# Optimization experiments

Measured on AMD Instinct MI355X. Metric: run time of the kernel, lower is better.

Reference implementation:

```python
import jax, jax.numpy as jnp
import numpy as np

T_TYPES = 4      # node types
N_NODES = 8192   # nodes per type
D_IN = 256       # init_dim
H = 256          # hidden_dim
D_OUT = 64       # out_dim
N_LAYERS = 2     # args.trans_num
TEMP = 1.0       # args.search_temp


def _conv1d(x, w, b):
    # x: [T, N, Din] -> Conv1d over node axis (torch: data[j].T -> Conv1d -> .T)
    # w: [Dout, Din, 3], b: [Dout]
    y = jax.lax.conv_general_dilated(
        jnp.swapaxes(x, 1, 2), w, window_strides=(1,), padding=((1, 1),),
        dimension_numbers=('NCH', 'OIH', 'NCH'))
    return jnp.swapaxes(y + b[None, :, None], 1, 2)  # [T, N, Dout]


def _rel_conv1d(x, w, b):
    # per-type conv kernels: w [T, Dout, Din, 3], b [T, Dout]
    return jax.vmap(lambda xi, wi, bi: _conv1d(xi[None], wi, bi)[0])(x, w, b)


def setup_inputs() -> dict:
    key = jax.random.key(0)
    ks = jax.random.split(key, 16)
    s = 1.0 / np.sqrt(H)  # keep relu chains numerically tame
    return {
        'x': jax.random.normal(ks[0], (T_TYPES, N_NODES, D_IN), jnp.float32),
        'lin1_w': jax.random.normal(ks[1], (D_IN, H), jnp.float32) * s,
        'lin1_b': jax.random.normal(ks[2], (H,), jnp.float32) * 0.01,
        'lin_w': jax.random.normal(ks[3], (N_LAYERS, H, H), jnp.float32) * s,
        'lin_b': jax.random.normal(ks[4], (N_LAYERS, H), jnp.float32) * 0.01,
        'rel_lin_w': jax.random.normal(ks[5], (N_LAYERS, T_TYPES, H, H), jnp.float32) * s,
        'rel_lin_b': jax.random.normal(ks[6], (N_LAYERS, T_TYPES, H), jnp.float32) * 0.01,
        'conv_w': jax.random.normal(ks[7], (N_LAYERS, H, H, 3), jnp.float32) * s,
        'conv_b': jax.random.normal(ks[8], (N_LAYERS, H), jnp.float32) * 0.01,
        'rel_conv_w': jax.random.normal(ks[9], (N_LAYERS, T_TYPES, H, H, 3), jnp.float32) * s,
        'rel_conv_b': jax.random.normal(ks[10], (N_LAYERS, T_TYPES, H), jnp.float32) * 0.01,
        'out_w': jax.random.normal(ks[11], (H, D_OUT), jnp.float32) * s,
        'out_b': jax.random.normal(ks[12], (D_OUT,), jnp.float32) * 0.01,
        'trans_arch': jax.random.normal(ks[13], (N_LAYERS, 5), jnp.float32),
        'agg_arch': jax.random.normal(ks[14], (3,), jnp.float32),
    }


def reference(x, lin1_w, lin1_b, lin_w, lin_b, rel_lin_w, rel_lin_b,
              conv_w, conv_b, rel_conv_w, rel_conv_b, out_w, out_b,
              trans_arch, agg_arch):
    relu = jax.nn.relu
    tw = jax.nn.softmax(trans_arch / TEMP, axis=-1)  # [L, 5]
    aw = jax.nn.softmax(agg_arch / TEMP)             # [3]

    # input projection (lin1)
    h = jnp.einsum('tnd,de->tne', x, lin1_w) + lin1_b  # [T, N, H]

    for l in range(N_LAYERS):
        # TRANS_OPTION = ['linear','rel-linear','conv','rel-conv','identity']
        o_lin = relu(jnp.einsum('tnd,de->tne', h, lin_w[l]) + lin_b[l])
        o_rlin = relu(jnp.einsum('tnd,tde->tne', h, rel_lin_w[l]) + rel_lin_b[l][:, None, :])
        o_conv = relu(_conv1d(h, conv_w[l], conv_b[l]))
        o_rconv = relu(_rel_conv1d(h, rel_conv_w[l], rel_conv_b[l]))
        w = tw[l]
        h = w[0] * o_lin + w[1] * o_rlin + w[2] * o_conv + w[3] * o_rconv + w[4] * h

    # Agg_Op: concat all types along node axis, AGG_OPTION = ['sum','mean','max']
    flat = h.reshape(-1, H)  # [T*N, H]
    agg = aw[0] * flat.sum(axis=0) + aw[1] * flat.mean(axis=0) + aw[2] * flat.max(axis=0)

    # reconstructed output head (class body truncated in source)
    return agg @ out_w + out_b  # [D_OUT]
```

## Files before the change

### kernel.cpp

```cpp
#include <hip/hip_runtime.h>
#include <hip/hip_bf16.h>
#include <math.h>

#define NN 8192
#define HP 8194
#define HD 256
#define DOUT 64

typedef __bf16 bf16_t;
typedef __bf16 bf16x8 __attribute__((ext_vector_type(8)));
typedef float f32x4 __attribute__((ext_vector_type(4)));

#define H0_OFF 0ull
#define H1_OFF 16781312ull
#define PW_OFF 33562624ull
#define TW_OFF 38936576ull
#define PS_OFF 38936832ull
#define PM_OFF 39198976ull
#define PWG_L1 0
#define PWG_SH(l) (8192 + (l)*32768)
#define PWG_TY(l) (73728 + (l)*131072)

__device__ __forceinline__ void glds16(const void* g, void* l) {
    __builtin_amdgcn_global_load_lds(
        (const __attribute__((address_space(1))) void*)g,
        (__attribute__((address_space(3))) void*)l, 16, 0, 0);
}

__device__ __forceinline__ float frelu(float v) { return v > 0.f ? v : 0.f; }

__global__ __launch_bounds__(256) void pack_kernel(
    const float* __restrict__ lin1_w, const float* __restrict__ lin_w,
    const float* __restrict__ rel_lin_w, const float* __restrict__ conv_w,
    const float* __restrict__ rel_conv_w, const float* __restrict__ trans_arch,
    const float* __restrict__ agg_arch, bf16_t* __restrict__ pw,
    float* __restrict__ tws, bf16_t* __restrict__ h0, bf16_t* __restrict__ h1) {
    const int bxi = blockIdx.x;
    if (bxi < 1312) {
        int g = bxi * 256 + threadIdx.x;
        int lrow = g & 15, lq = (g >> 4) & 3, j2 = (g >> 6) & 3;
        float v[8];
        if (g < 8192) {
            int ct = (g >> 8) & 3, kt = g >> 10;
            int k = kt * 32 + lq * 8, n = ct * 64 + j2 * 16 + lrow;
#pragma unroll
            for (int e = 0; e < 8; ++e) v[e] = lin1_w[(k + e) * 256 + n];
        } else if (g < 73728) {
            int u = g - 8192; int l = u >> 15; int r = u & 32767;
            int s = (r >> 8) & 3, ct = (r >> 10) & 3, kt = r >> 12;
            int k = kt * 32 + lq * 8, n = ct * 64 + j2 * 16 + lrow;
            if (s == 0) {
#pragma unroll
                for (int e = 0; e < 8; ++e) v[e] = lin_w[(l * 256 + k + e) * 256 + n];
            } else {
#pragma unroll
                for (int e = 0; e < 8; ++e)
                    v[e] = conv_w[((l * 256 + n) * 256 + k + e) * 3 + (s - 1)];
            }
        } else {
            int u = g - 73728; int lt = u >> 15; int l = lt >> 2, tt = lt & 3;
            int r = u & 32767;
            int s = (r >> 8) & 3, ct = (r >> 10) & 3, kt = r >> 12;
            int k = kt * 32 + lq * 8, n = ct * 64 + j2 * 16 + lrow;
            if (s == 0) {
#pragma unroll
                for (int e = 0; e < 8; ++e)
                    v[e] = rel_lin_w[((l * 4 + tt) * 256 + k + e) * 256 + n];
            } else {
#pragma unroll
                for (int e = 0; e < 8; ++e)
                    v[e] = rel_conv_w[(((l * 4 + tt) * 256 + n) * 256 + k + e) * 3 + (s - 1)];
            }
        }
        bf16x8 wv;
#pragma unroll
        for (int e = 0; e < 8; ++e) wv[e] = (bf16_t)v[e];
        *(bf16x8*)(pw + (size_t)g * 8) = wv;
    } else if (bxi == 1312) {
        for (int idx = threadIdx.x; idx < 4096; idx += 256) {
            int row_id = idx >> 8, col = idx & 255;
            int buf = row_id >> 3, t_ = (row_id >> 1) & 3, side = row_id & 1;
            bf16_t* hb = buf ? h1 : h0;
            hb[((size_t)t_ * HP + (side ? (HP - 1) : 0)) * HD + col] = (bf16_t)0.f;
        }
    } else {
        if (threadIdx.x == 0) {
            for (int l = 0; l < 2; ++l) {
                float m = trans_arch[l * 5];
                for (int i = 1; i < 5; ++i) m = fmaxf(m, trans_arch[l * 5 + i]);
                float e[5], s = 0.f;
                for (int i = 0; i < 5; ++i) { e[i] = __expf(trans_arch[l * 5 + i] - m); s += e[i]; }
                for (int i = 0; i < 5; ++i) tws[l * 5 + i] = e[i] / s;
            }
            float m = fmaxf(fmaxf(agg_arch[0], agg_arch[1]), agg_arch[2]);
            float e0 = __expf(agg_arch[0] - m), e1 = __expf(agg_arch[1] - m), e2 = __expf(agg_arch[2] - m);
            float s = e0 + e1 + e2;
            tws[10] = e0 / s; tws[11] = e1 / s; tws[12] = e2 / s;
        }
    }
}

__device__ __forceinline__ void load_af(bf16x8 af[4], const bf16_t* lA,
                                        int sh, int wm, int lrow, int lq) {
#pragma unroll
    for (int i = 0; i < 4; ++i)
        af[i] = *(const bf16x8*)&lA[(sh + wm + i * 16 + lrow) * 40 + lq * 8];
}

__device__ __forceinline__ void do_mat(const bf16x8 af[4], const bf16_t* Bb,
                                       int grpbase, int lane, f32x4 acc[4][2]) {
#pragma unroll
    for (int j = 0; j < 2; ++j) {
        bf16x8 bfr = *(const bf16x8*)&Bb[(grpbase + j) * 512 + lane * 8];
#pragma unroll
        for (int i = 0; i < 4; ++i)
            acc[i][j] = __builtin_amdgcn_mfma_f32_16x16x32_bf16(af[i], bfr, acc[i][j], 0, 0, 0);
    }
}

__global__ __launch_bounds__(256, 2) void lin1_kernel(
    const float* __restrict__ x, bf16_t* __restrict__ h0,
    const bf16_t* __restrict__ pwL1, const float* __restrict__ b) {
    __shared__ __align__(16) bf16_t lA[128 * 40];
    __shared__ __align__(16) bf16_t lB[2][2048];
    const int tid = threadIdx.x, lane = tid & 63, wid = tid >> 6;
    const int bx = blockIdx.x;
    const int t = bx >> 8, rb = bx & 255, mt = rb >> 2, ct = rb & 3;
    const int m0 = mt * 128, c0 = ct * 64;
    const int wm = (wid >> 1) * 64, wn = (wid & 1) * 32;
    const int lrow = lane & 15, lq = lane >> 4;
    const int wj2 = wn >> 4;
    const int r0 = tid >> 1, kq0 = (tid & 1) * 2;
    const float* xT = x + (size_t)t * NN * HD + (size_t)(m0 + r0) * HD + kq0 * 8;

    f32x4 acc[4][2];
#pragma unroll
    for (int i = 0; i < 4; ++i)
#pragma unroll
        for (int j = 0; j < 2; ++j) acc[i][j] = (f32x4){0.f, 0.f, 0.f, 0.f};

    float4 xa0, xa1, xa2, xa3;
    {
        const float4* p = (const float4*)(xT);
        xa0 = p[0]; xa1 = p[1]; xa2 = p[2]; xa3 = p[3];
    }
    {
        const bf16_t* src = pwL1 + (size_t)((0 * 4 + ct) * 4 + wid) * 512 + (size_t)lane * 8;
        glds16(src, &lB[0][wid * 512]);
    }
    for (int kt = 0; kt < 8; ++kt) {
        bf16x8 w0, w1;
        w0[0]=(bf16_t)xa0.x; w0[1]=(bf16_t)xa0.y; w0[2]=(bf16_t)xa0.z; w0[3]=(bf16_t)xa0.w;
        w0[4]=(bf16_t)xa1.x; w0[5]=(bf16_t)xa1.y; w0[6]=(bf16_t)xa1.z; w0[7]=(bf16_t)xa1.w;
        w1[0]=(bf16_t)xa2.x; w1[1]=(bf16_t)xa2.y; w1[2]=(bf16_t)xa2.z; w1[3]=(bf16_t)xa2.w;
        w1[4]=(bf16_t)xa3.x; w1[5]=(bf16_t)xa3.y; w1[6]=(bf16_t)xa3.z; w1[7]=(bf16_t)xa3.w;
        *(bf16x8*)&lA[r0 * 40 + kq0 * 8] = w0;
        *(bf16x8*)&lA[r0 * 40 + kq0 * 8 + 8] = w1;
        if (kt < 7) {
            const float4* p = (const float4*)(xT + (kt + 1) * 32);
            xa0 = p[0]; xa1 = p[1]; xa2 = p[2]; xa3 = p[3];
        }
        __syncthreads();
        if (kt < 7) {
            const bf16_t* src = pwL1 + (size_t)(((kt + 1) * 4 + ct) * 4 + wid) * 512 + (size_t)lane * 8;
            glds16(src, &lB[(kt + 1) & 1][wid * 512]);
        }
        const bf16_t* Bb = lB[kt & 1];
        bf16x8 af[4];
        load_af(af, lA, 0, wm, lrow, lq);
#pragma unroll
        for (int j = 0; j < 2; ++j) {
            bf16x8 bfr = *(const bf16x8*)&Bb[(wj2 + j) * 512 + lane * 8];
#pragma unroll
            for (int i = 0; i < 4; ++i)
                acc[i][j] = __builtin_amdgcn_mfma_f32_16x16x32_bf16(af[i], bfr, acc[i][j], 0, 0, 0);
        }
        __syncthreads();
    }
    size_t obase = (size_t)t * HP * HD + (size_t)(1 + m0) * HD;
#pragma unroll
    for (int j = 0; j < 2; ++j) {
        int col = c0 + wn + j * 16 + lrow;
        float bj = b[col];
#pragma unroll
        for (int i = 0; i < 4; ++i)
#pragma unroll
            for (int r = 0; r < 4; ++r) {
                int orow = wm + i * 16 + lq * 4 + r;
                h0[obase + (size_t)orow * HD + col] = (bf16_t)(acc[i][j][r] + bj);
            }
    }
}

__global__ __launch_bounds__(256, 2) void layer_kernel(
    const bf16_t* __restrict__ hin, bf16_t* __restrict__ hout,
    const bf16_t* __restrict__ pwS, const bf16_t* __restrict__ pwT,
    const float* __restrict__ lin_b, const float* __restrict__ rel_lin_b,
    const float* __restrict__ conv_b, const float* __restrict__ rel_conv_b,
    const float* __restrict__ tw5) {
    __shared__ __align__(16) bf16_t lA[130 * 40];
    __shared__ __align__(16) bf16_t lB[2][16384];
    const int tid = threadIdx.x, lane = tid & 63, wid = tid >> 6;
    const int bx = blockIdx.x;
    const int t = bx >> 8, rb = bx & 255, mt = rb >> 2, ct = rb & 3;
    const int m0 = mt * 128, c0 = ct * 64;
    const int wm = (wid >> 1) * 64, wn = (wid & 1) * 32;
    const int lrow = lane & 15, lq = lane >> 4;
    const int wj2 = wn >> 4;
    const bf16_t* aG = hin + (size_t)t * HP * HD + (size_t)m0 * HD;
    const bf16_t* pwTt = pwT + (size_t)t * 262144;
    const int r0 = tid >> 1, kq0 = (tid & 1) * 2;
    const int r1 = 128 + (tid >> 1);
    const bool tail = (tid < 4);

    f32x4 acc[4][4][2];
#pragma unroll
    for (int m = 0; m < 4; ++m)
#pragma unroll
        for (int i = 0; i < 4; ++i)
#pragma unroll
            for (int j = 0; j < 2; ++j) acc[m][i][j] = (f32x4){0.f, 0.f, 0.f, 0.f};

    bf16x8 pa0, pa1, pb0, pb1;
    pa0 = *(const bf16x8*)(aG + (size_t)r0 * HD + kq0 * 8);
    pa1 = *(const bf16x8*)(aG + (size_t)r0 * HD + kq0 * 8 + 8);
    if (tail) {
        pb0 = *(const bf16x8*)(aG + (size_t)r1 * HD + kq0 * 8);
        pb1 = *(const bf16x8*)(aG + (size_t)r1 * HD + kq0 * 8 + 8);
    }
#pragma unroll
    for (int q = 0; q < 8; ++q) {
        int tk = wid * 8 + q, half = tk >> 4, grp = tk & 15;
        const bf16_t* src = (half ? pwTt : pwS) + (size_t)((0 * 4 + ct) * 16 + grp) * 512 + (size_t)lane * 8;
        glds16(src, &lB[0][(half * 16 + grp) * 512]);
    }
    for (int kt = 0; kt < 8; ++kt) {
        *(bf16x8*)&lA[r0 * 40 + kq0 * 8] = pa0;
        *(bf16x8*)&lA[r0 * 40 + kq0 * 8 + 8] = pa1;
        if (tail) {
            *(bf16x8*)&lA[r1 * 40 + kq0 * 8] = pb0;
            *(bf16x8*)&lA[r1 * 40 + kq0 * 8 + 8] = pb1;
        }
        if (kt < 7) {
            pa0 = *(const bf16x8*)(aG + (size_t)r0 * HD + (kt + 1) * 32 + kq0 * 8);
            pa1 = *(const bf16x8*)(aG + (size_t)r0 * HD + (kt + 1) * 32 + kq0 * 8 + 8);
            if (tail) {
                pb0 = *(const bf16x8*)(aG + (size_t)r1 * HD + (kt + 1) * 32 + kq0 * 8);
                pb1 = *(const bf16x8*)(aG + (size_t)r1 * HD + (kt + 1) * 32 + kq0 * 8 + 8);
            }
        }
        __syncthreads();
        if (kt < 7) {
            int buf = (kt + 1) & 1;
#pragma unroll
            for (int q = 0; q < 8; ++q) {
                int tk = wid * 8 + q, half = tk >> 4, grp = tk & 15;
                const bf16_t* src = (half ? pwTt : pwS) + (size_t)(((kt + 1) * 4 + ct) * 16 + grp) * 512 + (size_t)lane * 8;
                glds16(src, &lB[buf][(half * 16 + grp) * 512]);
            }
        }
        const bf16_t* Bb = lB[kt & 1];
        bf16x8 af[4];
        load_af(af, lA, 1, wm, lrow, lq);
        do_mat(af, Bb, 0 + 0 + wj2, lane, acc[0]);
        do_mat(af, Bb, 16 + 0 + wj2, lane, acc[1]);
        do_mat(af, Bb, 0 + 8 + wj2, lane, acc[2]);
        do_mat(af, Bb, 16 + 8 + wj2, lane, acc[3]);
        load_af(af, lA, 0, wm, lrow, lq);
        do_mat(af, Bb, 0 + 4 + wj2, lane, acc[2]);
        do_mat(af, Bb, 16 + 4 + wj2, lane, acc[3]);
        load_af(af, lA, 2, wm, lrow, lq);
        do_mat(af, Bb, 0 + 12 + wj2, lane, acc[2]);
        do_mat(af, Bb, 16 + 12 + wj2, lane, acc[3]);
        __syncthreads();
    }
    const float w0 = tw5[0], w1 = tw5[1], w2 = tw5[2], w3 = tw5[3], w4 = tw5[4];
    const float* rb1 = rel_lin_b + t * 256;
    const float* rb3 = rel_conv_b + t * 256;
    size_t obase = (size_t)t * HP * HD + (size_t)(1 + m0) * HD;
#pragma unroll
    for (int j = 0; j < 2; ++j) {
        int col = c0 + wn + j * 16 + lrow;
        float b0 = lin_b[col], b1 = rb1[col], b2 = conv_b[col], b3 = rb3[col];
#pragma unroll
        for (int i = 0; i < 4; ++i)
#pragma unroll
            for (int r = 0; r < 4; ++r) {
                int orow = wm + i * 16 + lq * 4 + r;
                size_t idx = obase + (size_t)orow * HD + col;
                float v = w0 * frelu(acc[0][i][j][r] + b0)
                        + w1 * frelu(acc[1][i][j][r] + b1)
                        + w2 * frelu(acc[2][i][j][r] + b2)
                        + w3 * frelu(acc[3][i][j][r] + b3)
                        + w4 * (float)hin[idx];
                hout[idx] = (bf16_t)v;
            }
    }
}

__global__ __launch_bounds__(256) void reduce1_kernel(
    const bf16_t* __restrict__ h, float* __restrict__ ps, float* __restrict__ pm) {
    __shared__ float ss[2048], sm[2048];
    const int tid = threadIdx.x, b = blockIdx.x;
    const int t = b >> 6, rblk = b & 63;
    const int cg = tid & 31, rs = tid >> 5;
    const bf16_t* base = h + ((size_t)t * HP + 1 + rblk * 128) * HD + cg * 8;
    float s[8], m[8];
#pragma unroll
    for (int j = 0; j < 8; ++j) { s[j] = 0.f; m[j] = -3.4e38f; }
    for (int ii = 0; ii < 16; ++ii) {
        bf16x8 v = *(const bf16x8*)(base + (size_t)(rs + ii * 8) * HD);
#pragma unroll
        for (int j = 0; j < 8; ++j) {
            float f = (float)v[j];
            s[j] += f; m[j] = fmaxf(m[j], f);
        }
    }
#pragma unroll
    for (int j = 0; j < 8; ++j) { ss[rs * 256 + cg * 8 + j] = s[j]; sm[rs * 256 + cg * 8 + j] = m[j]; }
    __syncthreads();
    int c = tid;
    float S = 0.f, M = -3.4e38f;
#pragma unroll
    for (int r = 0; r < 8; ++r) { S += ss[r * 256 + c]; M = fmaxf(M, sm[r * 256 + c]); }
    ps[c * 256 + b] = S;
    pm[c * 256 + b] = M;
}

__global__ void reduce2_kernel(const float* __restrict__ ps, const float* __restrict__ pm,
                               const float* __restrict__ out_w, const float* __restrict__ out_b,
                               const float* __restrict__ tws, float* __restrict__ out) {
    __shared__ float aggL[256];
    int c = threadIdx.x;
    float s = 0.f, m = -3.4e38f;
    const float4* p4 = (const float4*)(ps + (size_t)c * 256);
    const float4* q4 = (const float4*)(pm + (size_t)c * 256);
    for (int i = 0; i < 64; ++i) {
        float4 a = p4[i]; s += a.x + a.y + a.z + a.w;
        float4 b = q4[i]; m = fmaxf(m, fmaxf(fmaxf(b.x, b.y), fmaxf(b.z, b.w)));
    }
    float aw0 = tws[10], aw1 = tws[11], aw2 = tws[12];
    aggL[c] = aw0 * s + aw1 * (s * (1.0f / 32768.f)) + aw2 * m;
    __syncthreads();
    if (c < DOUT) {
        float o = out_b[c];
        for (int e = 0; e < 256; ++e) o += aggL[e] * out_w[e * DOUT + c];
        out[c] = o;
    }
}

extern "C" void kernel_launch(void* const* d_in, const int* in_sizes, int n_in,
                              void* d_out, int out_size, void* d_ws, size_t ws_size,
                              hipStream_t stream) {
    const float* x          = (const float*)d_in[0];
    const float* lin1_w     = (const float*)d_in[1];
    const float* lin1_b     = (const float*)d_in[2];
    const float* lin_w      = (const float*)d_in[3];
    const float* lin_b      = (const float*)d_in[4];
    const float* rel_lin_w  = (const float*)d_in[5];
    const float* rel_lin_b  = (const float*)d_in[6];
    const float* conv_w     = (const float*)d_in[7];
    const float* conv_b     = (const float*)d_in[8];
    const float* rel_conv_w = (const float*)d_in[9];
    const float* rel_conv_b = (const float*)d_in[10];
    const float* out_w      = (const float*)d_in[11];
    const float* out_b      = (const float*)d_in[12];
    const float* trans_arch = (const float*)d_in[13];
    const float* agg_arch   = (const float*)d_in[14];

    char* ws = (char*)d_ws;
    bf16_t* h0 = (bf16_t*)(ws + H0_OFF);
    bf16_t* h1 = (bf16_t*)(ws + H1_OFF);
    bf16_t* pw = (bf16_t*)(ws + PW_OFF);
    float* tws = (float*)(ws + TW_OFF);
    float* ps  = (float*)(ws + PS_OFF);
    float* pm  = (float*)(ws + PM_OFF);
    float* outp = (float*)d_out;

    pack_kernel<<<1314, 256, 0, stream>>>(lin1_w, lin_w, rel_lin_w, conv_w, rel_conv_w,
                                          trans_arch, agg_arch, pw, tws, h0, h1);
    lin1_kernel<<<1024, 256, 0, stream>>>(x, h0, pw + (size_t)PWG_L1 * 8, lin1_b);
    layer_kernel<<<1024, 256, 0, stream>>>(h0, h1,
        pw + (size_t)PWG_SH(0) * 8, pw + (size_t)PWG_TY(0) * 8,
        lin_b, rel_lin_b, conv_b, rel_conv_b, tws);
    layer_kernel<<<1024, 256, 0, stream>>>(h1, h0,
        pw + (size_t)PWG_SH(1) * 8, pw + (size_t)PWG_TY(1) * 8,
        lin_b + 256, rel_lin_b + 1024, conv_b + 256, rel_conv_b + 1024, tws + 5);
    reduce1_kernel<<<256, 256, 0, stream>>>(h0, ps, pm);
    reduce2_kernel<<<1, 256, 0, stream>>>(ps, pm, out_w, out_b, tws, outp);
}
```

Before: 234.0 us.

## Fuse reduction into last layer, coalesce weight packing, restructure lin1 and buffering

Weight packing now stages tiles through shared memory so global reads are coalesced, replacing strided per-element gathers. This cuts the pack grid from 1314 blocks to 410. The lin1 kernel now computes a full 64x256 output tile per block, so x is read once rather than four times. The layer kernel drops LDS double-buffering to single-buffered B in order to raise occupancy to 3 blocks per CU, which exposes the weight load latency. The second layer also computes per-block column sums and maxes in its epilogue, removing the separate reduce1 pass over h.

After: 331.4 us. 41.6% more time.

```diff
diff --git a/kernel.cpp b/kernel.cpp
--- a/kernel.cpp
+++ b/kernel.cpp
@@ -35,56 +35,76 @@
     const float* __restrict__ rel_conv_w, const float* __restrict__ trans_arch,
     const float* __restrict__ agg_arch, bf16_t* __restrict__ pw,
     float* __restrict__ tws, bf16_t* __restrict__ h0, bf16_t* __restrict__ h1) {
-    const int bxi = blockIdx.x;
-    if (bxi < 1312) {
-        int g = bxi * 256 + threadIdx.x;
-        int lrow = g & 15, lq = (g >> 4) & 3, j2 = (g >> 6) & 3;
-        float v[8];
-        if (g < 8192) {
-            int ct = (g >> 8) & 3, kt = g >> 10;
-            int k = kt * 32 + lq * 8, n = ct * 64 + j2 * 16 + lrow;
-#pragma unroll
-            for (int e = 0; e < 8; ++e) v[e] = lin1_w[(k + e) * 256 + n];
-        } else if (g < 73728) {
-            int u = g - 8192; int l = u >> 15; int r = u & 32767;
-            int s = (r >> 8) & 3, ct = (r >> 10) & 3, kt = r >> 12;
-            int k = kt * 32 + lq * 8, n = ct * 64 + j2 * 16 + lrow;
-            if (s == 0) {
-#pragma unroll
-                for (int e = 0; e < 8; ++e) v[e] = lin_w[(l * 256 + k + e) * 256 + n];
-            } else {
-#pragma unroll
-                for (int e = 0; e < 8; ++e)
-                    v[e] = conv_w[((l * 256 + n) * 256 + k + e) * 3 + (s - 1)];
-            }
-        } else {
-            int u = g - 73728; int lt = u >> 15; int l = lt >> 2, tt = lt & 3;
-            int r = u & 32767;
-            int s = (r >> 8) & 3, ct = (r >> 10) & 3, kt = r >> 12;
-            int k = kt * 32 + lq * 8, n = ct * 64 + j2 * 16 + lrow;
-            if (s == 0) {
-#pragma unroll
-                for (int e = 0; e < 8; ++e)
-                    v[e] = rel_lin_w[((l * 4 + tt) * 256 + k + e) * 256 + n];
-            } else {
-#pragma unroll
-                for (int e = 0; e < 8; ++e)
-                    v[e] = rel_conv_w[(((l * 4 + tt) * 256 + n) * 256 + k + e) * 3 + (s - 1)];
-            }
-        }
-        bf16x8 wv;
-#pragma unroll
-        for (int e = 0; e < 8; ++e) wv[e] = (bf16_t)v[e];
-        *(bf16x8*)(pw + (size_t)g * 8) = wv;
-    } else if (bxi == 1312) {
-        for (int idx = threadIdx.x; idx < 4096; idx += 256) {
-            int row_id = idx >> 8, col = idx & 255;
+    __shared__ float lt[32 * 257];
+    const int tid = threadIdx.x, bx = blockIdx.x;
+    if (bx < 88) {
+        int m = bx >> 3, kt = bx & 7;
+        const float* src; size_t img; bool l1 = (m == 0);
+        if (m == 0) { src = lin1_w; img = 0; }
+        else if (m <= 2) { int l = m - 1; src = lin_w + (size_t)l * 65536; img = PWG_SH(l); }
+        else { int u = m - 3; int l = u >> 2, tt = u & 3;
+            src = rel_lin_w + (size_t)(l * 4 + tt) * 65536;
+            img = PWG_TY(l) + (size_t)tt * 32768; }
+        const float4* s4 = (const float4*)(src + (size_t)kt * 32 * 256);
+#pragma unroll
+        for (int i = 0; i < 8; ++i) {
+            int idx = tid + 256 * i;
+            float4 v = s4[idx];
+            int k = idx >> 6, n = (idx * 4) & 255;
+            float* p = &lt[k * 257 + n];
+            p[0] = v.x; p[1] = v.y; p[2] = v.z; p[3] = v.w;
+        }
+        __syncthreads();
+        int j2 = tid >> 6, lq = (tid >> 4) & 3, lrow = tid & 15;
+#pragma unroll
+        for (int ct = 0; ct < 4; ++ct) {
+            int n = ct * 64 + j2 * 16 + lrow;
+            bf16x8 wv;
+#pragma unroll
+            for (int e = 0; e < 8; ++e) wv[e] = (bf16_t)lt[(lq * 8 + e) * 257 + n];
+            size_t g = l1 ? (img + (size_t)kt * 1024 + ct * 256 + tid)
+                          : (img + (size_t)kt * 4096 + ct * 1024 + tid);
+            *(bf16x8*)(pw + g * 8) = wv;
+        }
+    } else if (bx < 408) {
+        int idx = bx - 88;
+        int inst = idx >> 5, r = idx & 31, kt = r >> 2, ct = r & 3;
+        const float* src; size_t img;
+        if (inst < 2) { src = conv_w + (size_t)inst * 196608; img = PWG_SH(inst); }
+        else { int u = inst - 2; int l = u >> 2, tt = u & 3;
+            src = rel_conv_w + (size_t)(l * 4 + tt) * 196608;
+            img = PWG_TY(l) + (size_t)tt * 32768; }
+        {
+            int rl = tid >> 2, q0 = tid & 3;
+            int n = ct * 64 + rl;
+            const float4* rb = (const float4*)(src) + (size_t)n * 192 + kt * 24;
+#pragma unroll
+            for (int i = 0; i < 6; ++i) {
+                float4 v = rb[q0 + 4 * i];
+                float* p = &lt[rl * 100 + (q0 + 4 * i) * 4];
+                p[0] = v.x; p[1] = v.y; p[2] = v.z; p[3] = v.w;
+            }
+        }
+        __syncthreads();
+        int j2 = tid >> 6, lq = (tid >> 4) & 3, lrow = tid & 15;
+        int nl = j2 * 16 + lrow;
+#pragma unroll
+        for (int s = 1; s <= 3; ++s) {
+            bf16x8 wv;
+#pragma unroll
+            for (int e = 0; e < 8; ++e) wv[e] = (bf16_t)lt[nl * 100 + (lq * 8 + e) * 3 + (s - 1)];
+            size_t g = img + (size_t)kt * 4096 + ct * 1024 + s * 256 + tid;
+            *(bf16x8*)(pw + g * 8) = wv;
+        }
+    } else if (bx == 408) {
+        for (int i = tid; i < 4096; i += 256) {
+            int row_id = i >> 8, col = i & 255;
             int buf = row_id >> 3, t_ = (row_id >> 1) & 3, side = row_id & 1;
             bf16_t* hb = buf ? h1 : h0;
             hb[((size_t)t_ * HP + (side ? (HP - 1) : 0)) * HD + col] = (bf16_t)0.f;
         }
     } else {
-        if (threadIdx.x == 0) {
+        if (tid == 0) {
             for (int l = 0; l < 2; ++l) {
                 float m = trans_arch[l * 5];
                 for (int i = 1; i < 5; ++i) m = fmaxf(m, trans_arch[l * 5 + i]);
@@ -121,85 +141,78 @@
 __global__ __launch_bounds__(256, 2) void lin1_kernel(
     const float* __restrict__ x, bf16_t* __restrict__ h0,
     const bf16_t* __restrict__ pwL1, const float* __restrict__ b) {
-    __shared__ __align__(16) bf16_t lA[128 * 40];
-    __shared__ __align__(16) bf16_t lB[2][2048];
+    __shared__ __align__(16) bf16_t lA[64 * 40];
+    __shared__ __align__(16) bf16_t lB[8192];
     const int tid = threadIdx.x, lane = tid & 63, wid = tid >> 6;
     const int bx = blockIdx.x;
-    const int t = bx >> 8, rb = bx & 255, mt = rb >> 2, ct = rb & 3;
-    const int m0 = mt * 128, c0 = ct * 64;
-    const int wm = (wid >> 1) * 64, wn = (wid & 1) * 32;
+    const int t = bx >> 7, mt = bx & 127;
+    const int m0 = mt * 64;
     const int lrow = lane & 15, lq = lane >> 4;
-    const int wj2 = wn >> 4;
-    const int r0 = tid >> 1, kq0 = (tid & 1) * 2;
+    const int r0 = tid >> 2, kq0 = tid & 3;
     const float* xT = x + (size_t)t * NN * HD + (size_t)(m0 + r0) * HD + kq0 * 8;
 
-    f32x4 acc[4][2];
+    f32x4 acc[4][4];
 #pragma unroll
     for (int i = 0; i < 4; ++i)
 #pragma unroll
-        for (int j = 0; j < 2; ++j) acc[i][j] = (f32x4){0.f, 0.f, 0.f, 0.f};
-
-    float4 xa0, xa1, xa2, xa3;
-    {
-        const float4* p = (const float4*)(xT);
-        xa0 = p[0]; xa1 = p[1]; xa2 = p[2]; xa3 = p[3];
-    }
-    {
-        const bf16_t* src = pwL1 + (size_t)((0 * 4 + ct) * 4 + wid) * 512 + (size_t)lane * 8;
-        glds16(src, &lB[0][wid * 512]);
-    }
+        for (int j = 0; j < 4; ++j) acc[i][j] = (f32x4){0.f, 0.f, 0.f, 0.f};
+
+    float4 px0, px1;
+    { const float4* p = (const float4*)xT; px0 = p[0]; px1 = p[1]; }
+
     for (int kt = 0; kt < 8; ++kt) {
-        bf16x8 w0, w1;
-        w0[0]=(bf16_t)xa0.x; w0[1]=(bf16_t)xa0.y; w0[2]=(bf16_t)xa0.z; w0[3]=(bf16_t)xa0.w;
-        w0[4]=(bf16_t)xa1.x; w0[5]=(bf16_t)xa1.y; w0[6]=(bf16_t)xa1.z; w0[7]=(bf16_t)xa1.w;
-        w1[0]=(bf16_t)xa2.x; w1[1]=(bf16_t)xa2.y; w1[2]=(bf16_t)xa2.z; w1[3]=(bf16_t)xa2.w;
-        w1[4]=(bf16_t)xa3.x; w1[5]=(bf16_t)xa3.y; w1[6]=(bf16_t)xa3.z; w1[7]=(bf16_t)xa3.w;
-        *(bf16x8*)&lA[r0 * 40 + kq0 * 8] = w0;
-        *(bf16x8*)&lA[r0 * 40 + kq0 * 8 + 8] = w1;
+        __syncthreads();
+        bf16x8 wv;
+        wv[0]=(bf16_t)px0.x; wv[1]=(bf16_t)px0.y; wv[2]=(bf16_t)px0.z; wv[3]=(bf16_t)px0.w;
+        wv[4]=(bf16_t)px1.x; wv[5]=(bf16_t)px1.y; wv[6]=(bf16_t)px1.z; wv[7]=(bf16_t)px1.w;
+        *(bf16x8*)&lA[r0 * 40 + kq0 * 8] = wv;
+#pragma unroll
+        for (int j2 = 0; j2 < 4; ++j2) {
+            const bf16_t* src = pwL1 + ((size_t)kt * 1024 + wid * 256 + j2 * 64) * 8 + (size_t)lane * 8;
+            glds16(src, &lB[(wid * 4 + j2) * 512]);
+        }
         if (kt < 7) {
             const float4* p = (const float4*)(xT + (kt + 1) * 32);
-            xa0 = p[0]; xa1 = p[1]; xa2 = p[2]; xa3 = p[3];
-        }
-        __syncthreads();
-        if (kt < 7) {
-            const bf16_t* src = pwL1 + (size_t)(((kt + 1) * 4 + ct) * 4 + wid) * 512 + (size_t)lane * 8;
-            glds16(src, &lB[(kt + 1) & 1][wid * 512]);
-        }
-        const bf16_t* Bb = lB[kt & 1];
+            px0 = p[0]; px1 = p[1];
+        }
+        __syncthreads();
         bf16x8 af[4];
-        load_af(af, lA, 0, wm, lrow, lq);
-#pragma unroll
-        for (int j = 0; j < 2; ++j) {
-            bf16x8 bfr = *(const bf16x8*)&Bb[(wj2 + j) * 512 + lane * 8];
+#pragma unroll
+        for (int i = 0; i < 4; ++i)
+            af[i] = *(const bf16x8*)&lA[(i * 16 + lrow) * 40 + lq * 8];
+#pragma unroll
+        for (int j = 0; j < 4; ++j) {
+            bf16x8 bfr = *(const bf16x8*)&lB[(wid * 4 + j) * 512 + lane * 8];
 #pragma unroll
             for (int i = 0; i < 4; ++i)
                 acc[i][j] = __builtin_amdgcn_mfma_f32_16x16x32_bf16(af[i], bfr, acc[i][j], 0, 0, 0);
         }
-        __syncthreads();
     }
     size_t obase = (size_t)t * HP * HD + (size_t)(1 + m0) * HD;
 #pragma unroll
-    for (int j = 0; j < 2; ++j) {
-        int col = c0 + wn + j * 16 + lrow;
+    for (int j = 0; j < 4; ++j) {
+        int col = wid * 64 + j * 16 + lrow;
         float bj = b[col];
 #pragma unroll
         for (int i = 0; i < 4; ++i)
 #pragma unroll
             for (int r = 0; r < 4; ++r) {
-                int orow = wm + i * 16 + lq * 4 + r;
+                int orow = i * 16 + lq * 4 + r;
                 h0[obase + (size_t)orow * HD + col] = (bf16_t)(acc[i][j][r] + bj);
             }
     }
 }
 
-__global__ __launch_bounds__(256, 2) void layer_kernel(
+template <int DO_RED>
+__global__ __launch_bounds__(256, 3) void layer_kernel(
     const bf16_t* __restrict__ hin, bf16_t* __restrict__ hout,
     const bf16_t* __restrict__ pwS, const bf16_t* __restrict__ pwT,
     const float* __restrict__ lin_b, const float* __restrict__ rel_lin_b,
     const float* __restrict__ conv_b, const float* __restrict__ rel_conv_b,
-    const float* __restrict__ tw5) {
+    const float* __restrict__ tw5, float* __restrict__ ps, float* __restrict__ pm) {
     __shared__ __align__(16) bf16_t lA[130 * 40];
-    __shared__ __align__(16) bf16_t lB[2][16384];
+    __shared__ __align__(16) bf16_t lB[16384];
+    __shared__ float lsum[4][64], lmax[4][64];
     const int tid = threadIdx.x, lane = tid & 63, wid = tid >> 6;
     const int bx = blockIdx.x;
     const int t = bx >> 8, rb = bx & 255, mt = rb >> 2, ct = rb & 3;
@@ -228,18 +241,19 @@
         pb0 = *(const bf16x8*)(aG + (size_t)r1 * HD + kq0 * 8);
         pb1 = *(const bf16x8*)(aG + (size_t)r1 * HD + kq0 * 8 + 8);
     }
-#pragma unroll
-    for (int q = 0; q < 8; ++q) {
-        int tk = wid * 8 + q, half = tk >> 4, grp = tk & 15;
-        const bf16_t* src = (half ? pwTt : pwS) + (size_t)((0 * 4 + ct) * 16 + grp) * 512 + (size_t)lane * 8;
-        glds16(src, &lB[0][(half * 16 + grp) * 512]);
-    }
     for (int kt = 0; kt < 8; ++kt) {
+        __syncthreads();
         *(bf16x8*)&lA[r0 * 40 + kq0 * 8] = pa0;
         *(bf16x8*)&lA[r0 * 40 + kq0 * 8 + 8] = pa1;
         if (tail) {
             *(bf16x8*)&lA[r1 * 40 + kq0 * 8] = pb0;
             *(bf16x8*)&lA[r1 * 40 + kq0 * 8 + 8] = pb1;
+        }
+#pragma unroll
+        for (int q = 0; q < 8; ++q) {
+            int tk = wid * 8 + q, half = tk >> 4, grp = tk & 15;
+            const bf16_t* src = (half ? pwTt : pwS) + (size_t)((kt * 4 + ct) * 16 + grp) * 512 + (size_t)lane * 8;
+            glds16(src, &lB[(half * 16 + grp) * 512]);
         }
         if (kt < 7) {
             pa0 = *(const bf16x8*)(aG + (size_t)r0 * HD + (kt + 1) * 32 + kq0 * 8);
@@ -250,34 +264,26 @@
             }
         }
         __syncthreads();
-        if (kt < 7) {
-            int buf = (kt + 1) & 1;
-#pragma unroll
-            for (int q = 0; q < 8; ++q) {
-                int tk = wid * 8 + q, half = tk >> 4, grp = tk & 15;
-                const bf16_t* src = (half ? pwTt : pwS) + (size_t)(((kt + 1) * 4 + ct) * 16 + grp) * 512 + (size_t)lane * 8;
-                glds16(src, &lB[buf][(half * 16 + grp) * 512]);
-            }
-        }
-        const bf16_t* Bb = lB[kt & 1];
         bf16x8 af[4];
         load_af(af, lA, 1, wm, lrow, lq);
-        do_mat(af, Bb, 0 + 0 + wj2, lane, acc[0]);
-        do_mat(af, Bb, 16 + 0 + wj2, lane, acc[1]);
-        do_mat(af, Bb, 0 + 8 + wj2, lane, acc[2]);
-        do_mat(af, Bb, 16 + 8 + wj2, lane, acc[3]);
+        do_mat(af, lB, 0 + 0 + wj2, lane, acc[0]);
+        do_mat(af, lB, 16 + 0 + wj2, lane, acc[1]);
+        do_mat(af, lB, 0 + 8 + wj2, lane, acc[2]);
+        do_mat(af, lB, 16 + 8 + wj2, lane, acc[3]);
         load_af(af, lA, 0, wm, lrow, lq);
-        do_mat(af, Bb, 0 + 4 + wj2, lane, acc[2]);
-        do_mat(af, Bb, 16 + 4 + wj2, lane, acc[3]);
+        do_mat(af, lB, 0 + 4 + wj2, lane, acc[2]);
+        do_mat(af, lB, 16 + 4 + wj2, lane, acc[3]);
         load_af(af, lA, 2, wm, lrow, lq);
-        do_mat(af, Bb, 0 + 12 + wj2, lane, acc[2]);
-        do_mat(af, Bb, 16 + 12 + wj2, lane, acc[3]);
-        __syncthreads();
+        do_mat(af, lB, 0 + 12 + wj2, lane, acc[2]);
+        do_mat(af, lB, 16 + 12 + wj2, lane, acc[3]);
     }
     const float w0 = tw5[0], w1 = tw5[1], w2 = tw5[2], w3 = tw5[3], w4 = tw5[4];
     const float* rb1 = rel_lin_b + t * 256;
     const float* rb3 = rel_conv_b + t * 256;
     size_t obase = (size_t)t * HP * HD + (size_t)(1 + m0) * HD;
+    float csum[2], cmax[2];
+#pragma unroll
+    for (int j = 0; j < 2; ++j) { csum[j] = 0.f; cmax[j] = -3.4e38f; }
 #pragma unroll
     for (int j = 0; j < 2; ++j) {
         int col = c0 + wn + j * 16 + lrow;
@@ -294,37 +300,35 @@
                         + w3 * frelu(acc[3][i][j][r] + b3)
                         + w4 * (float)hin[idx];
                 hout[idx] = (bf16_t)v;
-            }
-    }
-}
-
-__global__ __launch_bounds__(256) void reduce1_kernel(
-    const bf16_t* __restrict__ h, float* __restrict__ ps, float* __restrict__ pm) {
-    __shared__ float ss[2048], sm[2048];
-    const int tid = threadIdx.x, b = blockIdx.x;
-    const int t = b >> 6, rblk = b & 63;
-    const int cg = tid & 31, rs = tid >> 5;
-    const bf16_t* base = h + ((size_t)t * HP + 1 + rblk * 128) * HD + cg * 8;
-    float s[8], m[8];
-#pragma unroll
-    for (int j = 0; j < 8; ++j) { s[j] = 0.f; m[j] = -3.4e38f; }
-    for (int ii = 0; ii < 16; ++ii) {
-        bf16x8 v = *(const bf16x8*)(base + (size_t)(rs + ii * 8) * HD);
-#pragma unroll
-        for (int j = 0; j < 8; ++j) {
-            float f = (float)v[j];
-            s[j] += f; m[j] = fmaxf(m[j], f);
-        }
-    }
-#pragma unroll
-    for (int j = 0; j < 8; ++j) { ss[rs * 256 + cg * 8 + j] = s[j]; sm[rs * 256 + cg * 8 + j] = m[j]; }
-    __syncthreads();
-    int c = tid;
-    float S = 0.f, M = -3.4e38f;
-#pragma unroll
-    for (int r = 0; r < 8; ++r) { S += ss[r * 256 + c]; M = fmaxf(M, sm[r * 256 + c]); }
-    ps[c * 256 + b] = S;
-    pm[c * 256 + b] = M;
+                if (DO_RED) { csum[j] += v; cmax[j] = fmaxf(cmax[j], v); }
+            }
+    }
+    if (DO_RED) {
+#pragma unroll
+        for (int j = 0; j < 2; ++j) {
+            csum[j] += __shfl_xor(csum[j], 16, 64);
+            csum[j] += __shfl_xor(csum[j], 32, 64);
+            float o1 = __shfl_xor(cmax[j], 16, 64); cmax[j] = fmaxf(cmax[j], o1);
+            float o2 = __shfl_xor(cmax[j], 32, 64); cmax[j] = fmaxf(cmax[j], o2);
+        }
+        __syncthreads();
+        if (lq == 0) {
+#pragma unroll
+            for (int j = 0; j < 2; ++j) {
+                lsum[wid][wn + j * 16 + lrow] = csum[j];
+                lmax[wid][wn + j * 16 + lrow] = cmax[j];
+            }
+        }
+        __syncthreads();
+        if (tid < 64) {
+            int w0i = tid >> 5;
+            float S = lsum[w0i][tid] + lsum[w0i + 2][tid];
+            float M = fmaxf(lmax[w0i][tid], lmax[w0i + 2][tid]);
+            int g = t * 64 + mt;
+            ps[g * 256 + c0 + tid] = S;
+            pm[g * 256 + c0 + tid] = M;
+        }
+    }
 }
 
 __global__ void reduce2_kernel(const float* __restrict__ ps, const float* __restrict__ pm,
@@ -333,11 +337,10 @@
     __shared__ float aggL[256];
     int c = threadIdx.x;
     float s = 0.f, m = -3.4e38f;
-    const float4* p4 = (const float4*)(ps + (size_t)c * 256);
-    const float4* q4 = (const float4*)(pm + (size_t)c * 256);
-    for (int i = 0; i < 64; ++i) {
-        float4 a = p4[i]; s += a.x + a.y + a.z + a.w;
-        float4 b = q4[i]; m = fmaxf(m, fmaxf(fmaxf(b.x, b.y), fmaxf(b.z, b.w)));
+#pragma unroll 8
+    for (int g = 0; g < 256; ++g) {
+        s += ps[g * 256 + c];
+        m = fmaxf(m, pm[g * 256 + c]);
     }
     float aw0 = tws[10], aw1 = tws[11], aw2 = tws[12];
     aggL[c] = aw0 * s + aw1 * (s * (1.0f / 32768.f)) + aw2 * m;
@@ -377,15 +380,14 @@
     float* pm  = (float*)(ws + PM_OFF);
     float* outp = (float*)d_out;
 
-    pack_kernel<<<1314, 256, 0, stream>>>(lin1_w, lin_w, rel_lin_w, conv_w, rel_conv_w,
-                                          trans_arch, agg_arch, pw, tws, h0, h1);
-    lin1_kernel<<<1024, 256, 0, stream>>>(x, h0, pw + (size_t)PWG_L1 * 8, lin1_b);
-    layer_kernel<<<1024, 256, 0, stream>>>(h0, h1,
+    pack_kernel<<<410, 256, 0, stream>>>(lin1_w, lin_w, rel_lin_w, conv_w, rel_conv_w,
+                                         trans_arch, agg_arch, pw, tws, h0, h1);
+    lin1_kernel<<<512, 256, 0, stream>>>(x, h0, pw + (size_t)PWG_L1 * 8, lin1_b);
+    layer_kernel<0><<<1024, 256, 0, stream>>>(h0, h1,
         pw + (size_t)PWG_SH(0) * 8, pw + (size_t)PWG_TY(0) * 8,
-        lin_b, rel_lin_b, conv_b, rel_conv_b, tws);
-    layer_kernel<<<1024, 256, 0, stream>>>(h1, h0,
+        lin_b, rel_lin_b, conv_b, rel_conv_b, tws, nullptr, nullptr);
+    layer_kernel<1><<<1024, 256, 0, stream>>>(h1, h0,
         pw + (size_t)PWG_SH(1) * 8, pw + (size_t)PWG_TY(1) * 8,
-        lin_b + 256, rel_lin_b + 1024, conv_b + 256, rel_conv_b + 1024, tws + 5);
-    reduce1_kernel<<<256, 256, 0, stream>>>(h0, ps, pm);
+        lin_b + 256, rel_lin_b + 1024, conv_b + 256, rel_conv_b + 1024, tws + 5, ps, pm);
     reduce2_kernel<<<1, 256, 0, stream>>>(ps, pm, out_w, out_b, tws, outp);
 }
```
